# Kernel tuning notes

Measured on AMD Instinct MI355X. Metric: run time of the kernel, lower is better.

The kernel has to match this reference:

```python
import jax, jax.numpy as jnp
import numpy as np

N_NODES = 50000
N_EDGES = 1600000
IN_DIM = 128
HID = 64
N_GRAPHS = 256


def gcn_conv(x, row, col, W, b, n_nodes):
    """PyG GCNConv: symmetric gcn_norm with self-loops, linear-then-aggregate."""
    h = x @ W  # [N, out]
    loop = jnp.arange(n_nodes, dtype=row.dtype)
    r = jnp.concatenate([row, loop])  # sources (messages from x[r])
    c = jnp.concatenate([col, loop])  # targets (aggregate at c)
    ew = jnp.ones(r.shape[0], dtype=x.dtype)
    deg = jax.ops.segment_sum(ew, c, num_segments=n_nodes)
    dinv = jnp.where(deg > 0, jax.lax.rsqrt(deg), 0.0).astype(x.dtype)
    norm = dinv[r] * dinv[c]  # [E+N]
    out = jax.ops.segment_sum(norm[:, None] * h[r], c, num_segments=n_nodes)
    return out + b


def global_mean_pool(x, batch, n_graphs):
    sums = jax.ops.segment_sum(x, batch, num_segments=n_graphs)
    cnt = jax.ops.segment_sum(jnp.ones(x.shape[0], x.dtype), batch, num_segments=n_graphs)
    return sums / jnp.clip(cnt, 1.0)[:, None]


def setup_inputs() -> dict:
    key = jax.random.key(0)
    ks = jax.random.split(key, 12)
    x = jax.random.normal(ks[0], (N_NODES, IN_DIM), dtype=jnp.float32)
    edge_index = jax.random.randint(ks[1], (2, N_EDGES), 0, N_NODES, dtype=jnp.int64)
    batch = jnp.sort(jax.random.randint(ks[2], (N_NODES,), 0, N_GRAPHS, dtype=jnp.int64))
    def glorot(k, shp):
        lim = float(np.sqrt(6.0 / (shp[0] + shp[1])))
        return jax.random.uniform(k, shp, jnp.float32, -lim, lim)
    return {
        "x": x,
        "edge_index": edge_index,
        "batch": batch,
        "W1": glorot(ks[3], (IN_DIM, HID)), "b1": jnp.zeros((HID,), jnp.float32),
        "W2": glorot(ks[4], (HID, HID)), "b2": jnp.zeros((HID,), jnp.float32),
        "W3": glorot(ks[5], (HID, HID)), "b3": jnp.zeros((HID,), jnp.float32),
        "Wl1": glorot(ks[6], (HID, 16)), "bl1": jnp.zeros((16,), jnp.float32),
        "Wl2": glorot(ks[7], (16, 1)), "bl2": jnp.zeros((1,), jnp.float32),
    }


def reference(x, edge_index, batch, W1, b1, W2, b2, W3, b3, Wl1, bl1, Wl2, bl2):
    n = x.shape[0]
    row, col = edge_index[0], edge_index[1]
    h = jax.nn.relu(gcn_conv(x, row, col, W1, b1, n))
    h = jax.nn.relu(gcn_conv(h, row, col, W2, b2, n))
    h = jax.nn.relu(gcn_conv(h, row, col, W3, b3, n))
    g = global_mean_pool(h, batch, N_GRAPHS)  # [G, 64]
    out = (g @ Wl1 + bl1) @ Wl2 + bl2  # [G, 1]
    return out
```

## Files before the change

### kernel.cpp

```cpp
#include <hip/hip_runtime.h>

#define HID 64
#define B1 512
#define NBMAX 200
#define CAP 10368
#define ENTCAP 3200
#define CPT 21
#define QBITS 3

typedef __attribute__((ext_vector_type(8))) short short8;
typedef __attribute__((ext_vector_type(4))) float float4v;
typedef float f32x2 __attribute__((ext_vector_type(2)));

__device__ __forceinline__ ushort f2bf(float f) {
  unsigned u = __float_as_uint(f);
  unsigned r = (u + 0x7fffu + ((u >> 16) & 1u)) >> 16;
  return (ushort)r;
}
__device__ __forceinline__ float bf2f(ushort v) {
  return __uint_as_float(((unsigned)v) << 16);
}

__device__ __forceinline__ void acc8(f32x2& a01, f32x2& a23, uint2 d) {
  f32x2 t0, t1;
  t0.x = __uint_as_float(d.x << 16);
  t0.y = __uint_as_float(d.x & 0xffff0000u);
  t1.x = __uint_as_float(d.y << 16);
  t1.y = __uint_as_float(d.y & 0xffff0000u);
  a01 += t0;
  a23 += t1;
}


__global__ __launch_bounds__(256) void bucket_hist(const int* __restrict__ col, int E, int epb,
                                                   int* __restrict__ blockcnt,
                                                   const float* __restrict__ W1,
                                                   const float* __restrict__ W2,
                                                   const float* __restrict__ W3,
                                                   ushort* __restrict__ Wt1h, ushort* __restrict__ Wt1l,
                                                   ushort* __restrict__ Wt2h, ushort* __restrict__ Wt2l,
                                                   ushort* __restrict__ Wt3h, ushort* __restrict__ Wt3l) {
  int b = blockIdx.x, t = threadIdx.x;
  int gt = b * 256 + t;
  if (gt < 128 * 64) {
    int k = gt >> 6, nn = gt & 63;
    float w = W1[gt];
    ushort h = f2bf(w);
    Wt1h[nn * 128 + k] = h;
    Wt1l[nn * 128 + k] = f2bf(w - bf2f(h));
  }
  if (gt < 64 * 64) {
    int k = gt >> 6, nn = gt & 63;
    float w2 = W2[gt], w3 = W3[gt];
    ushort h2 = f2bf(w2), h3 = f2bf(w3);
    Wt2h[nn * 64 + k] = h2;
    Wt2l[nn * 64 + k] = f2bf(w2 - bf2f(h2));
    Wt3h[nn * 64 + k] = h3;
    Wt3l[nn * 64 + k] = f2bf(w3 - bf2f(h3));
  }

  __shared__ int cnt[256];
  cnt[t] = 0;
  __syncthreads();
  int lo = b * epb, hi = min(lo + epb, E);
  int ecnt = hi - lo;
  if (ecnt > 0) {
    int ecnt4 = ecnt & ~3;
    for (int i = t * 4; i < ecnt4; i += 1024) {
      int4 c4 = *(const int4*)&col[lo + i];
      atomicAdd(&cnt[c4.x >> 8], 1);
      atomicAdd(&cnt[c4.y >> 8], 1);
      atomicAdd(&cnt[c4.z >> 8], 1);
      atomicAdd(&cnt[c4.w >> 8], 1);
    }
    for (int i = ecnt4 + t; i < ecnt; i += 256) atomicAdd(&cnt[col[lo + i] >> 8], 1);
  }
  __syncthreads();
  blockcnt[b * 256 + t] = cnt[t];
}

__global__ __launch_bounds__(512) void scan_blocks(int* __restrict__ blockcnt,
                                                   int* __restrict__ buckettot) {
  __shared__ int s[512];
  int k = blockIdx.x;
  int t = threadIdx.x;
  int v = blockcnt[t * 256 + k];
  s[t] = v;
  __syncthreads();
  for (int d = 1; d < 512; d <<= 1) {
    int u = (t >= d) ? s[t - d] : 0;
    __syncthreads();
    s[t] += u;
    __syncthreads();
  }
  blockcnt[t * 256 + k] = s[t] - v;
  if (t == 511) buckettot[k] = s[t];
}

__global__ __launch_bounds__(256) void scan_buckettot(const int* __restrict__ buckettot,
                                                      int* __restrict__ bucketbase,
                                                      int* __restrict__ csr_off, int n, int E,
                                                      int nb) {
  __shared__ int s[256];
  int t = threadIdx.x;
  int v = buckettot[t];
  s[t] = v;
  __syncthreads();
  for (int d = 1; d < 256; d <<= 1) {
    int u = (t >= d) ? s[t - d] : 0;
    __syncthreads();
    s[t] += u;
    __syncthreads();
  }
  bucketbase[t] = s[t] - v;
  if (t == 255) bucketbase[256] = s[255];
  if (t == 0) csr_off[n] = E;
}

__global__ __launch_bounds__(256) void bin_edges(const int* __restrict__ row,
                                                 const int* __restrict__ col, int E, int epb,
                                                 const int* __restrict__ blockcnt,
                                                 const int* __restrict__ bucketbase,
                                                 unsigned* __restrict__ binned) {
  __shared__ int cnt[256];
  __shared__ int ofs[256];
  __shared__ int gb[256];
  __shared__ int lcur[256];
  __shared__ unsigned ent[ENTCAP];
  __shared__ unsigned stage[ENTCAP];
  int b = blockIdx.x, t = threadIdx.x;
  int lo = b * epb, hi = min(lo + epb, E);
  int ecnt = hi - lo;

  cnt[t] = 0;
  __syncthreads();
  if (ecnt > 0) {
    int ecnt4 = ecnt & ~3;
    for (int i = t * 4; i < ecnt4; i += 1024) {
      int4 c4 = *(const int4*)&col[lo + i];
      int4 r4 = *(const int4*)&row[lo + i];
      uint4 e4;
      e4.x = ((unsigned)r4.x << 16) | (unsigned)c4.x;
      e4.y = ((unsigned)r4.y << 16) | (unsigned)c4.y;
      e4.z = ((unsigned)r4.z << 16) | (unsigned)c4.z;
      e4.w = ((unsigned)r4.w << 16) | (unsigned)c4.w;
      *(uint4*)&ent[i] = e4;
      atomicAdd(&cnt[c4.x >> 8], 1);
      atomicAdd(&cnt[c4.y >> 8], 1);
      atomicAdd(&cnt[c4.z >> 8], 1);
      atomicAdd(&cnt[c4.w >> 8], 1);
    }
    for (int i = ecnt4 + t; i < ecnt; i += 256) {
      int c = col[lo + i];
      int r = row[lo + i];
      ent[i] = ((unsigned)r << 16) | (unsigned)c;
      atomicAdd(&cnt[c >> 8], 1);
    }
  }
  __syncthreads();
  int v = cnt[t];
  ofs[t] = v;
  __syncthreads();
  for (int d = 1; d < 256; d <<= 1) {
    int u = (t >= d) ? ofs[t - d] : 0;
    __syncthreads();
    ofs[t] += u;
    __syncthreads();
  }
  int excl = ofs[t] - v;
  int g = bucketbase[t] + blockcnt[b * 256 + t];
  __syncthreads();
  ofs[t] = excl;
  gb[t] = g;
  lcur[t] = excl;
  __syncthreads();
  if (ecnt > 0) {
    for (int i = t; i < ecnt; i += 256) {
      unsigned en = ent[i];
      int p = atomicAdd(&lcur[(en >> 8) & 255], 1);
      stage[p] = en;
    }
  }
  __syncthreads();
  if (ecnt > 0) {
    for (int i = t; i < ecnt; i += 256) {
      unsigned en = stage[i];
      int bb = (en >> 8) & 255;
      binned[gb[bb] + (i - ofs[bb])] = en;
    }
  }
}

__global__ __launch_bounds__(512) void bucket_csr(const unsigned* __restrict__ binned,
                                                  const int* __restrict__ bucketbase,
                                                  int* __restrict__ csr_off,
                                                  int* __restrict__ csr_src,
                                                  float* __restrict__ dinv, int n) {
  __shared__ int cnt[256 << QBITS];
  __shared__ int sscan[512];
  __shared__ int lsrc[CAP];
  int k = blockIdx.x, t = threadIdx.x;
  int base = bucketbase[k], end = bucketbase[k + 1];
  int s = end - base;
  unsigned ent[CPT];
  cnt[t] = 0; cnt[512 + t] = 0; cnt[1024 + t] = 0; cnt[1536 + t] = 0;
  __syncthreads();
#pragma unroll
  for (int q = 0; q < CPT; ++q) {
    int i = q * 512 + t;
    if (i < s) {
      unsigned p = binned[base + i];
      ent[q] = p;
      atomicAdd(&cnt[((p & 255u) << QBITS) | ((p >> 29) & 7u)], 1);
    }
  }
  __syncthreads();
  int a0 = cnt[t * 4 + 0], a1 = cnt[t * 4 + 1], a2 = cnt[t * 4 + 2], a3 = cnt[t * 4 + 3];
  int tsum = a0 + a1 + a2 + a3;
  sscan[t] = tsum;
  __syncthreads();
  for (int d = 1; d < 512; d <<= 1) {
    int u = (t >= d) ? sscan[t - d] : 0;
    __syncthreads();
    sscan[t] += u;
    __syncthreads();
  }
  int ex = sscan[t] - tsum;
  cnt[t * 4 + 0] = ex;
  cnt[t * 4 + 1] = ex + a0;
  cnt[t * 4 + 2] = ex + a0 + a1;
  cnt[t * 4 + 3] = ex + a0 + a1 + a2;
  __syncthreads();
  if (t < 256) {
    int st = cnt[t << QBITS];
    int en2 = (t == 255) ? s : cnt[(t + 1) << QBITS];
    int node = (k << 8) + t;
    if (node < n) {
      csr_off[node] = base + st;
      dinv[node] = rsqrtf((float)(en2 - st + 1));
    }
  }
  __syncthreads();
#pragma unroll
  for (int q = 0; q < CPT; ++q) {
    int i = q * 512 + t;
    if (i < s) {
      unsigned p = ent[q];
      int pos = atomicAdd(&cnt[((p & 255u) << QBITS) | ((p >> 29) & 7u)], 1);
      if (pos < CAP) lsrc[pos] = (int)(p >> 16);
    }
  }
  __syncthreads();
  for (int i = t; i < s; i += 512) csr_src[base + i] = (i < CAP) ? lsrc[i] : 0;
}


template <int K>
__global__ __launch_bounds__(256) void gemm_mfma(const float* __restrict__ A,
                                                 const ushort* __restrict__ Wh,
                                                 const ushort* __restrict__ Wl,
                                                 const float* __restrict__ dinv,
                                                 ushort* __restrict__ out, int n) {
  int wave = (blockIdx.x * 256 + threadIdx.x) >> 6;
  int lane = threadIdx.x & 63;
  int row0 = wave * 16;
  if (row0 >= n) return;
  int m = lane & 15;
  int quad = lane >> 4;
  int r = row0 + m;
  int rc = (r < n) ? r : (n - 1);

  float4v acc[4];
#pragma unroll
  for (int t = 0; t < 4; ++t) acc[t] = (float4v){0.f, 0.f, 0.f, 0.f};

#pragma unroll
  for (int k0 = 0; k0 < K; k0 += 32) {
    const float4* xp = (const float4*)&A[(size_t)rc * K + k0 + quad * 8];
    float4 a0 = xp[0];
    float4 a1 = xp[1];
    float av[8] = {a0.x, a0.y, a0.z, a0.w, a1.x, a1.y, a1.z, a1.w};
    short8 ah, al;
#pragma unroll
    for (int i = 0; i < 8; ++i) {
      ushort h = f2bf(av[i]);
      ah[i] = (short)h;
      al[i] = (short)f2bf(av[i] - bf2f(h));
    }
#pragma unroll
    for (int t = 0; t < 4; ++t) {
      size_t wof = (size_t)(t * 16 + m) * K + k0 + quad * 8;
      short8 bh = *(const short8*)&Wh[wof];
      short8 bl = *(const short8*)&Wl[wof];
      acc[t] = __builtin_amdgcn_mfma_f32_16x16x32_bf16(ah, bh, acc[t], 0, 0, 0);
      acc[t] = __builtin_amdgcn_mfma_f32_16x16x32_bf16(al, bh, acc[t], 0, 0, 0);
      acc[t] = __builtin_amdgcn_mfma_f32_16x16x32_bf16(ah, bl, acc[t], 0, 0, 0);
    }
  }

  float4 dv = ((const float4*)dinv)[(row0 >> 2) + quad];
  float dvi[4] = {dv.x, dv.y, dv.z, dv.w};
#pragma unroll
  for (int i = 0; i < 4; ++i) {
    int orow = row0 + quad * 4 + i;
    if (orow < n) {
#pragma unroll
      for (int t = 0; t < 4; ++t) {
        out[(size_t)orow * 64 + t * 16 + m] = f2bf(dvi[i] * acc[t][i]);
      }
    }
  }
}


__global__ __launch_bounds__(256) void agg_kernel(
    const ushort* __restrict__ hs, const int* __restrict__ csr_off,
    const int* __restrict__ csr_src, const float* __restrict__ dinv,
    const float* __restrict__ bias, float* __restrict__ out, int n) {
  int wid = (blockIdx.x * 256 + threadIdx.x) >> 6;
  int lane = threadIdx.x & 63;
  if (wid >= n) return;
  int qe = lane >> 4;
  int fq = lane & 15;
  const uint2* hs2 = (const uint2*)hs;

  f32x2 a01 = {0.f, 0.f}, a23 = {0.f, 0.f};
  if (qe == 0) {
    acc8(a01, a23, hs2[(size_t)wid * 16 + fq]);
  }

  int j = csr_off[wid];
  int e = csr_off[wid + 1];

  int pre = min(e, (j + 3) & ~3);
  if (j + qe < pre) {
    int s0 = csr_src[j + qe];
    acc8(a01, a23, hs2[(size_t)s0 * 16 + fq]);
  }
  int base = pre;

  for (; base + 16 <= e; base += 16) {
    int4 s = *(const int4*)&csr_src[base + qe * 4];
    uint2 v0 = hs2[(size_t)s.x * 16 + fq];
    uint2 v1 = hs2[(size_t)s.y * 16 + fq];
    uint2 v2 = hs2[(size_t)s.z * 16 + fq];
    uint2 v3 = hs2[(size_t)s.w * 16 + fq];
    acc8(a01, a23, v0);
    acc8(a01, a23, v1);
    acc8(a01, a23, v2);
    acc8(a01, a23, v3);
  }

  for (; base + 4 <= e; base += 4) {
    int s0 = csr_src[base + qe];
    acc8(a01, a23, hs2[(size_t)s0 * 16 + fq]);
  }
  if (base + qe < e) {
    int s0 = csr_src[base + qe];
    acc8(a01, a23, hs2[(size_t)s0 * 16 + fq]);
  }

  a01.x += __shfl_xor(a01.x, 16, 64);
  a01.y += __shfl_xor(a01.y, 16, 64);
  a23.x += __shfl_xor(a23.x, 16, 64);
  a23.y += __shfl_xor(a23.y, 16, 64);
  a01.x += __shfl_xor(a01.x, 32, 64);
  a01.y += __shfl_xor(a01.y, 32, 64);
  a23.x += __shfl_xor(a23.x, 32, 64);
  a23.y += __shfl_xor(a23.y, 32, 64);

  if (qe == 0) {
    float d = dinv[wid];
    float4 bi = ((const float4*)bias)[fq];
    float4 r;
    r.x = fmaxf(d * a01.x + bi.x, 0.f);
    r.y = fmaxf(d * a01.y + bi.y, 0.f);
    r.z = fmaxf(d * a23.x + bi.z, 0.f);
    r.w = fmaxf(d * a23.y + bi.w, 0.f);
    ((float4*)out)[(size_t)wid * 16 + fq] = r;
  }
}


__global__ __launch_bounds__(256) void pool_mlp_kernel(
    const float* __restrict__ a, const int* __restrict__ batch, int n,
    const float* __restrict__ Wl1, const float* __restrict__ bl1,
    const float* __restrict__ Wl2, const float* __restrict__ bl2,
    float* __restrict__ out) {
  int g = blockIdx.x;
  int t = threadIdx.x;
  int lane = t & 63;
  int w = t >> 6;

  int lo = 0, hi = n;
  while (lo < hi) {
    int m = (lo + hi) >> 1;
    if (batch[m] < g) lo = m + 1; else hi = m;
  }
  int start = lo;
  lo = start; hi = n;
  while (lo < hi) {
    int m = (lo + hi) >> 1;
    if (batch[m] < g + 1) lo = m + 1; else hi = m;
  }
  int end = lo;

  float s = 0.f;
  for (int i = start + w; i < end; i += 4) s += a[i * 64 + lane];

  __shared__ float ps[4][64];
  __shared__ float gv[64];
  __shared__ float hv[16];
  ps[w][lane] = s;
  __syncthreads();
  if (w == 0) {
    float tot = ps[0][lane] + ps[1][lane] + ps[2][lane] + ps[3][lane];
    gv[lane] = tot / (float)max(end - start, 1);
  }
  __syncthreads();
  if (t < 16) {
    float h = bl1[t];
    for (int k = 0; k < 64; ++k) h += gv[k] * Wl1[k * 16 + t];
    hv[t] = h;
  }
  __syncthreads();
  if (t == 0) {
    float o = bl2[0];
    for (int j2 = 0; j2 < 16; ++j2) o += hv[j2] * Wl2[j2];
    out[g] = o;
  }
}


extern "C" void kernel_launch(void* const* d_in, const int* in_sizes, int n_in,
                              void* d_out, int out_size, void* d_ws, size_t ws_size,
                              hipStream_t stream) {
  const float* x = (const float*)d_in[0];
  const int* ei = (const int*)d_in[1];
  const int* batch = (const int*)d_in[2];
  const float* W1 = (const float*)d_in[3];
  const float* b1 = (const float*)d_in[4];
  const float* W2 = (const float*)d_in[5];
  const float* b2 = (const float*)d_in[6];
  const float* W3 = (const float*)d_in[7];
  const float* b3 = (const float*)d_in[8];
  const float* Wl1 = (const float*)d_in[9];
  const float* bl1 = (const float*)d_in[10];
  const float* Wl2 = (const float*)d_in[11];
  const float* bl2 = (const float*)d_in[12];

  int n = in_sizes[0] / 128;
  int E = in_sizes[1] / 2;
  int G = out_size;
  int nb = (n + 255) >> 8;
  int epb = (((E + B1 - 1) / B1) + 15) & ~15;

  const int* row = ei;
  const int* col = ei + E;

  char* p = (char*)d_ws;
  int* blockcnt = (int*)p;    p += B1 * 256 * 4;
  int* buckettot = (int*)p;   p += 256 * 4;
  int* bucketbase = (int*)p;  p += 272 * 4;
  int* csr_off = (int*)p;     p += 50064 * 4;
  float* dinv = (float*)p;    p += 50016 * 4;
  ushort* Wt1h = (ushort*)p;  p += 128 * 64 * 2;
  ushort* Wt1l = (ushort*)p;  p += 128 * 64 * 2;
  ushort* Wt2h = (ushort*)p;  p += 64 * 64 * 2;
  ushort* Wt2l = (ushort*)p;  p += 64 * 64 * 2;
  ushort* Wt3h = (ushort*)p;  p += 64 * 64 * 2;
  ushort* Wt3l = (ushort*)p;  p += 64 * 64 * 2;
  int* csr_src = (int*)p;     p += (size_t)((E + 15) / 16 * 16) * 4;
  ushort* hs = (ushort*)p;    p += (size_t)n * 64 * 2;
  float* abuf = (float*)p;
  unsigned* binned = (unsigned*)hs;

  bucket_hist<<<B1, 256, 0, stream>>>(col, E, epb, blockcnt,
                                      W1, W2, W3, Wt1h, Wt1l, Wt2h, Wt2l, Wt3h, Wt3l);
  scan_blocks<<<256, 512, 0, stream>>>(blockcnt, buckettot);
  scan_buckettot<<<1, 256, 0, stream>>>(buckettot, bucketbase, csr_off, n, E, nb);
  bin_edges<<<B1, 256, 0, stream>>>(row, col, E, epb, blockcnt, bucketbase, binned);
  bucket_csr<<<nb, 512, 0, stream>>>(binned, bucketbase, csr_off, csr_src, dinv, n);

  int nwaves = (n + 15) / 16;
  int gblocks = (nwaves + 3) / 4;
  int ablocks = (n * 64 + 255) / 256;

  gemm_mfma<128><<<gblocks, 256, 0, stream>>>(x, Wt1h, Wt1l, dinv, hs, n);
  agg_kernel<<<ablocks, 256, 0, stream>>>(hs, csr_off, csr_src, dinv, b1, abuf, n);
  gemm_mfma<64><<<gblocks, 256, 0, stream>>>(abuf, Wt2h, Wt2l, dinv, hs, n);
  agg_kernel<<<ablocks, 256, 0, stream>>>(hs, csr_off, csr_src, dinv, b2, abuf, n);
  gemm_mfma<64><<<gblocks, 256, 0, stream>>>(abuf, Wt3h, Wt3l, dinv, hs, n);
  agg_kernel<<<ablocks, 256, 0, stream>>>(hs, csr_off, csr_src, dinv, b3, abuf, n);
  pool_mlp_kernel<<<G, 256, 0, stream>>>(abuf, batch, n, Wl1, bl1, Wl2, bl2, (float*)d_out);
}
```

Before: 304.0 us.

## Split hidden features into two half buffers and drop bucket scan launch

The bf16 hidden features now go into two separate halves of 32 columns each. The aggregation kernel is launched with twice as many blocks, and each block gathers only one half per node, so every gathered row is a compact 64-byte segment and each half buffer has a smaller cache footprint. The single-block bucket-total scan kernel is removed, and its prefix scan is recomputed redundantly inside the bin_edges and bucket_csr blocks, saving one launch. In exchange, csr_src is read twice per layer and every block does extra scan work.

```diff
diff --git a/kernel.cpp b/kernel.cpp
--- a/kernel.cpp
+++ b/kernel.cpp
@@ -2,7 +2,6 @@
 
 #define HID 64
 #define B1 512
-#define NBMAX 200
 #define CAP 10368
 #define ENTCAP 3200
 #define CPT 21
@@ -97,30 +96,10 @@
   if (t == 511) buckettot[k] = s[t];
 }
 
-__global__ __launch_bounds__(256) void scan_buckettot(const int* __restrict__ buckettot,
-                                                      int* __restrict__ bucketbase,
-                                                      int* __restrict__ csr_off, int n, int E,
-                                                      int nb) {
-  __shared__ int s[256];
-  int t = threadIdx.x;
-  int v = buckettot[t];
-  s[t] = v;
-  __syncthreads();
-  for (int d = 1; d < 256; d <<= 1) {
-    int u = (t >= d) ? s[t - d] : 0;
-    __syncthreads();
-    s[t] += u;
-    __syncthreads();
-  }
-  bucketbase[t] = s[t] - v;
-  if (t == 255) bucketbase[256] = s[255];
-  if (t == 0) csr_off[n] = E;
-}
-
 __global__ __launch_bounds__(256) void bin_edges(const int* __restrict__ row,
                                                  const int* __restrict__ col, int E, int epb,
                                                  const int* __restrict__ blockcnt,
-                                                 const int* __restrict__ bucketbase,
+                                                 const int* __restrict__ buckettot,
                                                  unsigned* __restrict__ binned) {
   __shared__ int cnt[256];
   __shared__ int ofs[256];
@@ -131,6 +110,18 @@
   int b = blockIdx.x, t = threadIdx.x;
   int lo = b * epb, hi = min(lo + epb, E);
   int ecnt = hi - lo;
+
+  int bt = buckettot[t];
+  ofs[t] = bt;
+  __syncthreads();
+  for (int d = 1; d < 256; d <<= 1) {
+    int u = (t >= d) ? ofs[t - d] : 0;
+    __syncthreads();
+    ofs[t] += u;
+    __syncthreads();
+  }
+  int bb = ofs[t] - bt;
+  __syncthreads();
 
   cnt[t] = 0;
   __syncthreads();
@@ -168,7 +159,7 @@
     __syncthreads();
   }
   int excl = ofs[t] - v;
-  int g = bucketbase[t] + blockcnt[b * 256 + t];
+  int g = bb + blockcnt[b * 256 + t];
   __syncthreads();
   ofs[t] = excl;
   gb[t] = g;
@@ -185,14 +176,14 @@
   if (ecnt > 0) {
     for (int i = t; i < ecnt; i += 256) {
       unsigned en = stage[i];
-      int bb = (en >> 8) & 255;
-      binned[gb[bb] + (i - ofs[bb])] = en;
+      int bk = (en >> 8) & 255;
+      binned[gb[bk] + (i - ofs[bk])] = en;
     }
   }
 }
 
 __global__ __launch_bounds__(512) void bucket_csr(const unsigned* __restrict__ binned,
-                                                  const int* __restrict__ bucketbase,
+                                                  const int* __restrict__ buckettot,
                                                   int* __restrict__ csr_off,
                                                   int* __restrict__ csr_src,
                                                   float* __restrict__ dinv, int n) {
@@ -200,7 +191,21 @@
   __shared__ int sscan[512];
   __shared__ int lsrc[CAP];
   int k = blockIdx.x, t = threadIdx.x;
-  int base = bucketbase[k], end = bucketbase[k + 1];
+
+  int tot = (t < 256) ? buckettot[t] : 0;
+  sscan[t] = tot;
+  __syncthreads();
+  for (int d = 1; d < 512; d <<= 1) {
+    int u = (t >= d) ? sscan[t - d] : 0;
+    __syncthreads();
+    sscan[t] += u;
+    __syncthreads();
+  }
+  int base = (k == 0) ? 0 : sscan[k - 1];
+  int end = sscan[k];
+  if (k == 0 && t == 0) csr_off[n] = sscan[255];
+  __syncthreads();
+
   int s = end - base;
   unsigned ent[CPT];
   cnt[t] = 0; cnt[512 + t] = 0; cnt[1024 + t] = 0; cnt[1536 + t] = 0;
@@ -260,7 +265,8 @@
                                                  const ushort* __restrict__ Wh,
                                                  const ushort* __restrict__ Wl,
                                                  const float* __restrict__ dinv,
-                                                 ushort* __restrict__ out, int n) {
+                                                 ushort* __restrict__ lo,
+                                                 ushort* __restrict__ hi, int n) {
   int wave = (blockIdx.x * 256 + threadIdx.x) >> 6;
   int lane = threadIdx.x & 63;
   int row0 = wave * 16;
@@ -306,7 +312,8 @@
     if (orow < n) {
 #pragma unroll
       for (int t = 0; t < 4; ++t) {
-        out[(size_t)orow * 64 + t * 16 + m] = f2bf(dvi[i] * acc[t][i]);
+        ushort* dst = (t < 2) ? lo : hi;
+        dst[(size_t)orow * 32 + (t & 1) * 16 + m] = f2bf(dvi[i] * acc[t][i]);
       }
     }
   }
@@ -314,52 +321,59 @@
 
 
 __global__ __launch_bounds__(256) void agg_kernel(
-    const ushort* __restrict__ hs, const int* __restrict__ csr_off,
-    const int* __restrict__ csr_src, const float* __restrict__ dinv,
-    const float* __restrict__ bias, float* __restrict__ out, int n) {
-  int wid = (blockIdx.x * 256 + threadIdx.x) >> 6;
+    const ushort* __restrict__ hs_lo, const ushort* __restrict__ hs_hi,
+    const int* __restrict__ csr_off, const int* __restrict__ csr_src,
+    const float* __restrict__ dinv, const float* __restrict__ bias,
+    float* __restrict__ out, int n, int nwb) {
+  int bid = blockIdx.x;
+  int fh = (bid >= nwb) ? 1 : 0;
+  int wid = ((bid - fh * nwb) * 256 + threadIdx.x) >> 6;
   int lane = threadIdx.x & 63;
   if (wid >= n) return;
-  int qe = lane >> 4;
-  int fq = lane & 15;
-  const uint2* hs2 = (const uint2*)hs;
+  int qe = lane >> 3;
+  int fl = lane & 7;
+  const uint2* hs2 = (const uint2*)(fh ? hs_hi : hs_lo);
 
   f32x2 a01 = {0.f, 0.f}, a23 = {0.f, 0.f};
   if (qe == 0) {
-    acc8(a01, a23, hs2[(size_t)wid * 16 + fq]);
+    acc8(a01, a23, hs2[(size_t)wid * 8 + fl]);
   }
 
   int j = csr_off[wid];
   int e = csr_off[wid + 1];
 
-  int pre = min(e, (j + 3) & ~3);
+  int pre = min(e, (j + 7) & ~7);
   if (j + qe < pre) {
     int s0 = csr_src[j + qe];
-    acc8(a01, a23, hs2[(size_t)s0 * 16 + fq]);
+    acc8(a01, a23, hs2[(size_t)s0 * 8 + fl]);
   }
   int base = pre;
 
-  for (; base + 16 <= e; base += 16) {
+  for (; base + 32 <= e; base += 32) {
     int4 s = *(const int4*)&csr_src[base + qe * 4];
-    uint2 v0 = hs2[(size_t)s.x * 16 + fq];
-    uint2 v1 = hs2[(size_t)s.y * 16 + fq];
-    uint2 v2 = hs2[(size_t)s.z * 16 + fq];
-    uint2 v3 = hs2[(size_t)s.w * 16 + fq];
+    uint2 v0 = hs2[(size_t)s.x * 8 + fl];
+    uint2 v1 = hs2[(size_t)s.y * 8 + fl];
+    uint2 v2 = hs2[(size_t)s.z * 8 + fl];
+    uint2 v3 = hs2[(size_t)s.w * 8 + fl];
     acc8(a01, a23, v0);
     acc8(a01, a23, v1);
     acc8(a01, a23, v2);
     acc8(a01, a23, v3);
   }
 
-  for (; base + 4 <= e; base += 4) {
+  for (; base + 8 <= e; base += 8) {
     int s0 = csr_src[base + qe];
-    acc8(a01, a23, hs2[(size_t)s0 * 16 + fq]);
+    acc8(a01, a23, hs2[(size_t)s0 * 8 + fl]);
   }
   if (base + qe < e) {
     int s0 = csr_src[base + qe];
-    acc8(a01, a23, hs2[(size_t)s0 * 16 + fq]);
-  }
-
+    acc8(a01, a23, hs2[(size_t)s0 * 8 + fl]);
+  }
+
+  a01.x += __shfl_xor(a01.x, 8, 64);
+  a01.y += __shfl_xor(a01.y, 8, 64);
+  a23.x += __shfl_xor(a23.x, 8, 64);
+  a23.y += __shfl_xor(a23.y, 8, 64);
   a01.x += __shfl_xor(a01.x, 16, 64);
   a01.y += __shfl_xor(a01.y, 16, 64);
   a23.x += __shfl_xor(a23.x, 16, 64);
@@ -371,13 +385,13 @@
 
   if (qe == 0) {
     float d = dinv[wid];
-    float4 bi = ((const float4*)bias)[fq];
+    float4 bi = ((const float4*)bias)[fh * 8 + fl];
     float4 r;
     r.x = fmaxf(d * a01.x + bi.x, 0.f);
     r.y = fmaxf(d * a01.y + bi.y, 0.f);
     r.z = fmaxf(d * a23.x + bi.z, 0.f);
     r.w = fmaxf(d * a23.y + bi.w, 0.f);
-    ((float4*)out)[(size_t)wid * 16 + fq] = r;
+    ((float4*)out)[(size_t)wid * 16 + fh * 8 + fl] = r;
   }
 }
 
@@ -461,7 +475,6 @@
   char* p = (char*)d_ws;
   int* blockcnt = (int*)p;    p += B1 * 256 * 4;
   int* buckettot = (int*)p;   p += 256 * 4;
-  int* bucketbase = (int*)p;  p += 272 * 4;
   int* csr_off = (int*)p;     p += 50064 * 4;
   float* dinv = (float*)p;    p += 50016 * 4;
   ushort* Wt1h = (ushort*)p;  p += 128 * 64 * 2;
@@ -471,26 +484,27 @@
   ushort* Wt3h = (ushort*)p;  p += 64 * 64 * 2;
   ushort* Wt3l = (ushort*)p;  p += 64 * 64 * 2;
   int* csr_src = (int*)p;     p += (size_t)((E + 15) / 16 * 16) * 4;
-  ushort* hs = (ushort*)p;    p += (size_t)n * 64 * 2;
+  ushort* hsbuf = (ushort*)p; p += (size_t)n * 64 * 2;
   float* abuf = (float*)p;
-  unsigned* binned = (unsigned*)hs;
+  ushort* hs_lo = hsbuf;
+  ushort* hs_hi = hsbuf + (size_t)n * 32;
+  unsigned* binned = (unsigned*)hsbuf;
 
   bucket_hist<<<B1, 256, 0, stream>>>(col, E, epb, blockcnt,
                                       W1, W2, W3, Wt1h, Wt1l, Wt2h, Wt2l, Wt3h, Wt3l);
   scan_blocks<<<256, 512, 0, stream>>>(blockcnt, buckettot);
-  scan_buckettot<<<1, 256, 0, stream>>>(buckettot, bucketbase, csr_off, n, E, nb);
-  bin_edges<<<B1, 256, 0, stream>>>(row, col, E, epb, blockcnt, bucketbase, binned);
-  bucket_csr<<<nb, 512, 0, stream>>>(binned, bucketbase, csr_off, csr_src, dinv, n);
+  bin_edges<<<B1, 256, 0, stream>>>(row, col, E, epb, blockcnt, buckettot, binned);
+  bucket_csr<<<nb, 512, 0, stream>>>(binned, buckettot, csr_off, csr_src, dinv, n);
 
   int nwaves = (n + 15) / 16;
   int gblocks = (nwaves + 3) / 4;
-  int ablocks = (n * 64 + 255) / 256;
-
-  gemm_mfma<128><<<gblocks, 256, 0, stream>>>(x, Wt1h, Wt1l, dinv, hs, n);
-  agg_kernel<<<ablocks, 256, 0, stream>>>(hs, csr_off, csr_src, dinv, b1, abuf, n);
-  gemm_mfma<64><<<gblocks, 256, 0, stream>>>(abuf, Wt2h, Wt2l, dinv, hs, n);
-  agg_kernel<<<ablocks, 256, 0, stream>>>(hs, csr_off, csr_src, dinv, b2, abuf, n);
-  gemm_mfma<64><<<gblocks, 256, 0, stream>>>(abuf, Wt3h, Wt3l, dinv, hs, n);
-  agg_kernel<<<ablocks, 256, 0, stream>>>(hs, csr_off, csr_src, dinv, b3, abuf, n);
+  int nwb = (n + 3) / 4;
+
+  gemm_mfma<128><<<gblocks, 256, 0, stream>>>(x, Wt1h, Wt1l, dinv, hs_lo, hs_hi, n);
+  agg_kernel<<<2 * nwb, 256, 0, stream>>>(hs_lo, hs_hi, csr_off, csr_src, dinv, b1, abuf, n, nwb);
+  gemm_mfma<64><<<gblocks, 256, 0, stream>>>(abuf, Wt2h, Wt2l, dinv, hs_lo, hs_hi, n);
+  agg_kernel<<<2 * nwb, 256, 0, stream>>>(hs_lo, hs_hi, csr_off, csr_src, dinv, b2, abuf, n, nwb);
+  gemm_mfma<64><<<gblocks, 256, 0, stream>>>(abuf, Wt3h, Wt3l, dinv, hs_lo, hs_hi, n);
+  agg_kernel<<<2 * nwb, 256, 0, stream>>>(hs_lo, hs_hi, csr_off, csr_src, dinv, b3, abuf, n, nwb);
   pool_mlp_kernel<<<G, 256, 0, stream>>>(abuf, batch, n, Wl1, bl1, Wl2, bl2, (float*)d_out);
 }
```

Result: slower. 362.7 us (+19.3%).

## Replace two-pass scan-based edge binning with atomic fixed-capacity bucket slots

Applied to the files above, without the earlier changes.

Removes the separate histogram and two scan kernels. Edges are now binned in a single pass: each block reserves space in fixed-capacity per-bucket regions (CAP slots each) using global atomics, and bucket_csr recomputes the bucket prefix from the atomic totals. This cuts kernel launches and one full read of the column array, at the cost of a memset, nondeterministic edge order within buckets, and reliance on no bucket exceeding CAP entries. It also requires the binned buffer (aliased onto hs) to hold 256*CAP entries.

```diff
diff --git a/kernel.cpp b/kernel.cpp
--- a/kernel.cpp
+++ b/kernel.cpp
@@ -2,7 +2,6 @@
 
 #define HID 64
 #define B1 512
-#define NBMAX 200
 #define CAP 10368
 #define ENTCAP 3200
 #define CPT 21
@@ -32,16 +31,25 @@
 }
 
 
-__global__ __launch_bounds__(256) void bucket_hist(const int* __restrict__ col, int E, int epb,
-                                                   int* __restrict__ blockcnt,
-                                                   const float* __restrict__ W1,
-                                                   const float* __restrict__ W2,
-                                                   const float* __restrict__ W3,
-                                                   ushort* __restrict__ Wt1h, ushort* __restrict__ Wt1l,
-                                                   ushort* __restrict__ Wt2h, ushort* __restrict__ Wt2l,
-                                                   ushort* __restrict__ Wt3h, ushort* __restrict__ Wt3l) {
+__global__ __launch_bounds__(256) void bin_direct(const int* __restrict__ row,
+                                                  const int* __restrict__ col, int E, int epb,
+                                                  int* __restrict__ woffglob,
+                                                  unsigned* __restrict__ binned,
+                                                  const float* __restrict__ W1,
+                                                  const float* __restrict__ W2,
+                                                  const float* __restrict__ W3,
+                                                  ushort* __restrict__ Wt1h, ushort* __restrict__ Wt1l,
+                                                  ushort* __restrict__ Wt2h, ushort* __restrict__ Wt2l,
+                                                  ushort* __restrict__ Wt3h, ushort* __restrict__ Wt3l) {
+  __shared__ int cnt[256];
+  __shared__ int ofs[256];
+  __shared__ int gb[256];
+  __shared__ int lcur[256];
+  __shared__ unsigned ent[ENTCAP];
+  __shared__ unsigned stage[ENTCAP];
   int b = blockIdx.x, t = threadIdx.x;
   int gt = b * 256 + t;
+
   if (gt < 128 * 64) {
     int k = gt >> 6, nn = gt & 63;
     float w = W1[gt];
@@ -59,76 +67,6 @@
     Wt3l[nn * 64 + k] = f2bf(w3 - bf2f(h3));
   }
 
-  __shared__ int cnt[256];
-  cnt[t] = 0;
-  __syncthreads();
-  int lo = b * epb, hi = min(lo + epb, E);
-  int ecnt = hi - lo;
-  if (ecnt > 0) {
-    int ecnt4 = ecnt & ~3;
-    for (int i = t * 4; i < ecnt4; i += 1024) {
-      int4 c4 = *(const int4*)&col[lo + i];
-      atomicAdd(&cnt[c4.x >> 8], 1);
-      atomicAdd(&cnt[c4.y >> 8], 1);
-      atomicAdd(&cnt[c4.z >> 8], 1);
-      atomicAdd(&cnt[c4.w >> 8], 1);
-    }
-    for (int i = ecnt4 + t; i < ecnt; i += 256) atomicAdd(&cnt[col[lo + i] >> 8], 1);
-  }
-  __syncthreads();
-  blockcnt[b * 256 + t] = cnt[t];
-}
-
-__global__ __launch_bounds__(512) void scan_blocks(int* __restrict__ blockcnt,
-                                                   int* __restrict__ buckettot) {
-  __shared__ int s[512];
-  int k = blockIdx.x;
-  int t = threadIdx.x;
-  int v = blockcnt[t * 256 + k];
-  s[t] = v;
-  __syncthreads();
-  for (int d = 1; d < 512; d <<= 1) {
-    int u = (t >= d) ? s[t - d] : 0;
-    __syncthreads();
-    s[t] += u;
-    __syncthreads();
-  }
-  blockcnt[t * 256 + k] = s[t] - v;
-  if (t == 511) buckettot[k] = s[t];
-}
-
-__global__ __launch_bounds__(256) void scan_buckettot(const int* __restrict__ buckettot,
-                                                      int* __restrict__ bucketbase,
-                                                      int* __restrict__ csr_off, int n, int E,
-                                                      int nb) {
-  __shared__ int s[256];
-  int t = threadIdx.x;
-  int v = buckettot[t];
-  s[t] = v;
-  __syncthreads();
-  for (int d = 1; d < 256; d <<= 1) {
-    int u = (t >= d) ? s[t - d] : 0;
-    __syncthreads();
-    s[t] += u;
-    __syncthreads();
-  }
-  bucketbase[t] = s[t] - v;
-  if (t == 255) bucketbase[256] = s[255];
-  if (t == 0) csr_off[n] = E;
-}
-
-__global__ __launch_bounds__(256) void bin_edges(const int* __restrict__ row,
-                                                 const int* __restrict__ col, int E, int epb,
-                                                 const int* __restrict__ blockcnt,
-                                                 const int* __restrict__ bucketbase,
-                                                 unsigned* __restrict__ binned) {
-  __shared__ int cnt[256];
-  __shared__ int ofs[256];
-  __shared__ int gb[256];
-  __shared__ int lcur[256];
-  __shared__ unsigned ent[ENTCAP];
-  __shared__ unsigned stage[ENTCAP];
-  int b = blockIdx.x, t = threadIdx.x;
   int lo = b * epb, hi = min(lo + epb, E);
   int ecnt = hi - lo;
 
@@ -168,7 +106,8 @@
     __syncthreads();
   }
   int excl = ofs[t] - v;
-  int g = bucketbase[t] + blockcnt[b * 256 + t];
+  int g = 0;
+  if (v > 0) g = atomicAdd(&woffglob[t], v);
   __syncthreads();
   ofs[t] = excl;
   gb[t] = g;
@@ -185,14 +124,14 @@
   if (ecnt > 0) {
     for (int i = t; i < ecnt; i += 256) {
       unsigned en = stage[i];
-      int bb = (en >> 8) & 255;
-      binned[gb[bb] + (i - ofs[bb])] = en;
+      int bk = (en >> 8) & 255;
+      binned[bk * CAP + gb[bk] + (i - ofs[bk])] = en;
     }
   }
 }
 
 __global__ __launch_bounds__(512) void bucket_csr(const unsigned* __restrict__ binned,
-                                                  const int* __restrict__ bucketbase,
+                                                  const int* __restrict__ woffglob,
                                                   int* __restrict__ csr_off,
                                                   int* __restrict__ csr_src,
                                                   float* __restrict__ dinv, int n) {
@@ -200,8 +139,22 @@
   __shared__ int sscan[512];
   __shared__ int lsrc[CAP];
   int k = blockIdx.x, t = threadIdx.x;
-  int base = bucketbase[k], end = bucketbase[k + 1];
-  int s = end - base;
+
+  int tot = (t < 256) ? woffglob[t] : 0;
+  sscan[t] = tot;
+  __syncthreads();
+  for (int d = 1; d < 512; d <<= 1) {
+    int u = (t >= d) ? sscan[t - d] : 0;
+    __syncthreads();
+    sscan[t] += u;
+    __syncthreads();
+  }
+  int base = (k == 0) ? 0 : sscan[k - 1];
+  int s = sscan[k] - base;
+  if (k == 0 && t == 0) csr_off[n] = sscan[255];
+  __syncthreads();
+
+  const unsigned* bk = &binned[(size_t)k * CAP];
   unsigned ent[CPT];
   cnt[t] = 0; cnt[512 + t] = 0; cnt[1024 + t] = 0; cnt[1536 + t] = 0;
   __syncthreads();
@@ -209,7 +162,7 @@
   for (int q = 0; q < CPT; ++q) {
     int i = q * 512 + t;
     if (i < s) {
-      unsigned p = binned[base + i];
+      unsigned p = bk[i];
       ent[q] = p;
       atomicAdd(&cnt[((p & 255u) << QBITS) | ((p >> 29) & 7u)], 1);
     }
@@ -459,9 +412,7 @@
   const int* col = ei + E;
 
   char* p = (char*)d_ws;
-  int* blockcnt = (int*)p;    p += B1 * 256 * 4;
-  int* buckettot = (int*)p;   p += 256 * 4;
-  int* bucketbase = (int*)p;  p += 272 * 4;
+  int* woffglob = (int*)p;    p += 256 * 4;
   int* csr_off = (int*)p;     p += 50064 * 4;
   float* dinv = (float*)p;    p += 50016 * 4;
   ushort* Wt1h = (ushort*)p;  p += 128 * 64 * 2;
@@ -475,12 +426,10 @@
   float* abuf = (float*)p;
   unsigned* binned = (unsigned*)hs;
 
-  bucket_hist<<<B1, 256, 0, stream>>>(col, E, epb, blockcnt,
-                                      W1, W2, W3, Wt1h, Wt1l, Wt2h, Wt2l, Wt3h, Wt3l);
-  scan_blocks<<<256, 512, 0, stream>>>(blockcnt, buckettot);
-  scan_buckettot<<<1, 256, 0, stream>>>(buckettot, bucketbase, csr_off, n, E, nb);
-  bin_edges<<<B1, 256, 0, stream>>>(row, col, E, epb, blockcnt, bucketbase, binned);
-  bucket_csr<<<nb, 512, 0, stream>>>(binned, bucketbase, csr_off, csr_src, dinv, n);
+  hipMemsetAsync(woffglob, 0, 256 * 4, stream);
+  bin_direct<<<B1, 256, 0, stream>>>(row, col, E, epb, woffglob, binned,
+                                     W1, W2, W3, Wt1h, Wt1l, Wt2h, Wt2l, Wt3h, Wt3l);
+  bucket_csr<<<nb, 512, 0, stream>>>(binned, woffglob, csr_off, csr_src, dinv, n);
 
   int nwaves = (n + 15) / 16;
   int gblocks = (nwaves + 3) / 4;
```

Result: slower. 318.9 us (+4.9%).

## Fuse aggregation with next layer's dense transform via per-wave shuffle GEMV

Applied to the files above, without the earlier changes.

Layers 2 and 3 now run aggregation, bias and ReLU, then multiply by the next weight matrix inside a single kernel. Each wave broadcasts its aggregated row with shuffles and does an fp32 64x64 matvec, reading W straight from global memory. This removes two MFMA GEMM launches, the fp32 intermediate buffer round-trip and the bf16 hi/lo weight split for W2/W3. In exchange it adds per-node shuffle and FMA work and repeated weight loads per wave, which rely on cache hits.

```diff
diff --git a/kernel.cpp b/kernel.cpp
--- a/kernel.cpp
+++ b/kernel.cpp
@@ -35,11 +35,8 @@
 __global__ __launch_bounds__(256) void bucket_hist(const int* __restrict__ col, int E, int epb,
                                                    int* __restrict__ blockcnt,
                                                    const float* __restrict__ W1,
-                                                   const float* __restrict__ W2,
-                                                   const float* __restrict__ W3,
-                                                   ushort* __restrict__ Wt1h, ushort* __restrict__ Wt1l,
-                                                   ushort* __restrict__ Wt2h, ushort* __restrict__ Wt2l,
-                                                   ushort* __restrict__ Wt3h, ushort* __restrict__ Wt3l) {
+                                                   ushort* __restrict__ Wt1h,
+                                                   ushort* __restrict__ Wt1l) {
   int b = blockIdx.x, t = threadIdx.x;
   int gt = b * 256 + t;
   if (gt < 128 * 64) {
@@ -48,15 +45,6 @@
     ushort h = f2bf(w);
     Wt1h[nn * 128 + k] = h;
     Wt1l[nn * 128 + k] = f2bf(w - bf2f(h));
-  }
-  if (gt < 64 * 64) {
-    int k = gt >> 6, nn = gt & 63;
-    float w2 = W2[gt], w3 = W3[gt];
-    ushort h2 = f2bf(w2), h3 = f2bf(w3);
-    Wt2h[nn * 64 + k] = h2;
-    Wt2l[nn * 64 + k] = f2bf(w2 - bf2f(h2));
-    Wt3h[nn * 64 + k] = h3;
-    Wt3l[nn * 64 + k] = f2bf(w3 - bf2f(h3));
   }
 
   __shared__ int cnt[256];
@@ -310,6 +298,87 @@
       }
     }
   }
+}
+
+
+__global__ __launch_bounds__(256) void agg_gemm(
+    const ushort* __restrict__ hs_in, const int* __restrict__ csr_off,
+    const int* __restrict__ csr_src, const float* __restrict__ dinv,
+    const float* __restrict__ bias, const float* __restrict__ W,
+    ushort* __restrict__ hs_out, int n) {
+  int wid = (blockIdx.x * 256 + threadIdx.x) >> 6;
+  int lane = threadIdx.x & 63;
+  if (wid >= n) return;
+  int qe = lane >> 4;
+  int fq = lane & 15;
+  const uint2* hs2 = (const uint2*)hs_in;
+
+  f32x2 a01 = {0.f, 0.f}, a23 = {0.f, 0.f};
+  if (qe == 0) {
+    acc8(a01, a23, hs2[(size_t)wid * 16 + fq]);
+  }
+
+  int j = csr_off[wid];
+  int e = csr_off[wid + 1];
+
+  int pre = min(e, (j + 3) & ~3);
+  if (j + qe < pre) {
+    int s0 = csr_src[j + qe];
+    acc8(a01, a23, hs2[(size_t)s0 * 16 + fq]);
+  }
+  int base = pre;
+
+  for (; base + 16 <= e; base += 16) {
+    int4 s = *(const int4*)&csr_src[base + qe * 4];
+    uint2 v0 = hs2[(size_t)s.x * 16 + fq];
+    uint2 v1 = hs2[(size_t)s.y * 16 + fq];
+    uint2 v2 = hs2[(size_t)s.z * 16 + fq];
+    uint2 v3 = hs2[(size_t)s.w * 16 + fq];
+    acc8(a01, a23, v0);
+    acc8(a01, a23, v1);
+    acc8(a01, a23, v2);
+    acc8(a01, a23, v3);
+  }
+
+  for (; base + 4 <= e; base += 4) {
+    int s0 = csr_src[base + qe];
+    acc8(a01, a23, hs2[(size_t)s0 * 16 + fq]);
+  }
+  if (base + qe < e) {
+    int s0 = csr_src[base + qe];
+    acc8(a01, a23, hs2[(size_t)s0 * 16 + fq]);
+  }
+
+  a01.x += __shfl_xor(a01.x, 16, 64);
+  a01.y += __shfl_xor(a01.y, 16, 64);
+  a23.x += __shfl_xor(a23.x, 16, 64);
+  a23.y += __shfl_xor(a23.y, 16, 64);
+  a01.x += __shfl_xor(a01.x, 32, 64);
+  a01.y += __shfl_xor(a01.y, 32, 64);
+  a23.x += __shfl_xor(a23.x, 32, 64);
+  a23.y += __shfl_xor(a23.y, 32, 64);
+
+  float dd = dinv[wid];
+  float4 bi = ((const float4*)bias)[fq];
+  float r0 = fmaxf(dd * a01.x + bi.x, 0.f);
+  float r1 = fmaxf(dd * a01.y + bi.y, 0.f);
+  float r2 = fmaxf(dd * a23.x + bi.z, 0.f);
+  float r3 = fmaxf(dd * a23.y + bi.w, 0.f);
+
+  float h0 = 0.f, h1 = 0.f, h2 = 0.f, h3 = 0.f;
+#pragma unroll
+  for (int kq = 0; kq < 16; ++kq) {
+    float f0 = __shfl(r0, kq, 64);
+    float f1 = __shfl(r1, kq, 64);
+    float f2 = __shfl(r2, kq, 64);
+    float f3 = __shfl(r3, kq, 64);
+    h0 += f0 * W[(kq * 4 + 0) * 64 + lane];
+    h1 += f1 * W[(kq * 4 + 1) * 64 + lane];
+    h2 += f2 * W[(kq * 4 + 2) * 64 + lane];
+    h3 += f3 * W[(kq * 4 + 3) * 64 + lane];
+  }
+  float h = (h0 + h1) + (h2 + h3);
+  hs_out[(size_t)wid * 64 + lane] = f2bf(dd * h);
 }
 
 
@@ -466,17 +535,13 @@
   float* dinv = (float*)p;    p += 50016 * 4;
   ushort* Wt1h = (ushort*)p;  p += 128 * 64 * 2;
   ushort* Wt1l = (ushort*)p;  p += 128 * 64 * 2;
-  ushort* Wt2h = (ushort*)p;  p += 64 * 64 * 2;
-  ushort* Wt2l = (ushort*)p;  p += 64 * 64 * 2;
-  ushort* Wt3h = (ushort*)p;  p += 64 * 64 * 2;
-  ushort* Wt3l = (ushort*)p;  p += 64 * 64 * 2;
   int* csr_src = (int*)p;     p += (size_t)((E + 15) / 16 * 16) * 4;
-  ushort* hs = (ushort*)p;    p += (size_t)n * 64 * 2;
+  ushort* hs_a = (ushort*)p;  p += (size_t)n * 64 * 2;
+  ushort* hs_b = (ushort*)p;  p += (size_t)n * 64 * 2;
   float* abuf = (float*)p;
-  unsigned* binned = (unsigned*)hs;
-
-  bucket_hist<<<B1, 256, 0, stream>>>(col, E, epb, blockcnt,
-                                      W1, W2, W3, Wt1h, Wt1l, Wt2h, Wt2l, Wt3h, Wt3l);
+  unsigned* binned = (unsigned*)hs_a;
+
+  bucket_hist<<<B1, 256, 0, stream>>>(col, E, epb, blockcnt, W1, Wt1h, Wt1l);
   scan_blocks<<<256, 512, 0, stream>>>(blockcnt, buckettot);
   scan_buckettot<<<1, 256, 0, stream>>>(buckettot, bucketbase, csr_off, n, E, nb);
   bin_edges<<<B1, 256, 0, stream>>>(row, col, E, epb, blockcnt, bucketbase, binned);
@@ -486,11 +551,9 @@
   int gblocks = (nwaves + 3) / 4;
   int ablocks = (n * 64 + 255) / 256;
 
-  gemm_mfma<128><<<gblocks, 256, 0, stream>>>(x, Wt1h, Wt1l, dinv, hs, n);
-  agg_kernel<<<ablocks, 256, 0, stream>>>(hs, csr_off, csr_src, dinv, b1, abuf, n);
-  gemm_mfma<64><<<gblocks, 256, 0, stream>>>(abuf, Wt2h, Wt2l, dinv, hs, n);
-  agg_kernel<<<ablocks, 256, 0, stream>>>(hs, csr_off, csr_src, dinv, b2, abuf, n);
-  gemm_mfma<64><<<gblocks, 256, 0, stream>>>(abuf, Wt3h, Wt3l, dinv, hs, n);
-  agg_kernel<<<ablocks, 256, 0, stream>>>(hs, csr_off, csr_src, dinv, b3, abuf, n);
+  gemm_mfma<128><<<gblocks, 256, 0, stream>>>(x, Wt1h, Wt1l, dinv, hs_a, n);
+  agg_gemm<<<ablocks, 256, 0, stream>>>(hs_a, csr_off, csr_src, dinv, b1, W2, hs_b, n);
+  agg_gemm<<<ablocks, 256, 0, stream>>>(hs_b, csr_off, csr_src, dinv, b2, W3, hs_a, n);
+  agg_kernel<<<ablocks, 256, 0, stream>>>(hs_a, csr_off, csr_src, dinv, b3, abuf, n);
   pool_mlp_kernel<<<G, 256, 0, stream>>>(abuf, batch, n, Wl1, bl1, Wl2, bl2, (float*)d_out);
 }
```

Result: no change. 300.8 us (median of 2 runs) (-1.1%).
